# Performance work log

Measured on AMD Instinct MI355X. Metric: run time of the kernel, lower is better.

Reference implementation:

```python
import math
import jax, jax.numpy as jnp
import numpy as np

B, N, D, H = 4, 2048, 512, 8
HD = D // H


def setup_inputs() -> dict:
    key = jax.random.key(0)
    ks = jax.random.split(key, 7)
    w_scale = 1.0 / math.sqrt(D)  # keep logits in a sane range (like default init)
    return {
        "q": jax.random.normal(ks[0], (B, N, D), dtype=jnp.float32),
        "mask": jax.random.randint(ks[1], (B, N), 0, 2) == 1,  # True = masked key
        "attn_bias": jax.random.normal(ks[2], (B, N, N), dtype=jnp.float32),
        "Wq": jax.random.normal(ks[3], (D, D), dtype=jnp.float32) * w_scale,
        "Wk": jax.random.normal(ks[4], (D, D), dtype=jnp.float32) * w_scale,
        "Wv": jax.random.normal(ks[5], (D, D), dtype=jnp.float32) * w_scale,
        "Wo": jax.random.normal(ks[6], (D, D), dtype=jnp.float32) * w_scale,
    }


def _heads(v):
    # [B, N, D] -> [H, B, N, HD]  (mirrors reshape + movedim(-2, 0))
    b, n, d = v.shape
    return v.reshape(b, n, H, HD).transpose(2, 0, 1, 3)


def reference(q, mask, attn_bias, Wq, Wk, Wv, Wo):
    # Linear projections (torch Linear: x @ W.T)
    qh = _heads(q @ Wq.T)
    kh = _heads(q @ Wk.T)   # self-attention: h defaults to q
    vh = _heads(q @ Wv.T)
    # scores: [H, B, Nq, Nk]
    scores = jnp.einsum("hbqd,hbkd->hbqk", qh, kh) / math.sqrt(HD)
    scores = scores + attn_bias[None]                     # broadcast over heads
    scores = jnp.where(mask[None, :, None, :], -jnp.inf, scores)
    attn = jax.nn.softmax(scores, axis=-1)
    out = jnp.einsum("hbqk,hbkd->hbqd", attn, vh)         # [H, B, Nq, HD]
    out = out.transpose(1, 2, 0, 3).reshape(q.shape[0], q.shape[1], D)
    return out @ Wo.T
```

## Files before the change

kernel.cpp:

```cpp
#include <hip/hip_runtime.h>
#include <stdint.h>


typedef __attribute__((ext_vector_type(8))) short short8;
typedef __attribute__((ext_vector_type(4))) short short4v;
typedef __attribute__((ext_vector_type(4))) float f32x4;

#define DEV static __device__ __forceinline__

constexpr int Bc = 4, Nc = 2048, Dc = 512, Hc = 8, HDc = 64;
constexpr int Mc = Bc * Nc;
constexpr int QKVNc = 3 * Dc;
constexpr float L2E = 1.44269504f;

DEV short bf16cast(float f) {
  return (short)__builtin_bit_cast(unsigned short, (__bf16)f);
}
DEV unsigned cvt_pk_bf16(float a, float b) {
  unsigned short lb = __builtin_bit_cast(unsigned short, (__bf16)a);
  unsigned short hb = __builtin_bit_cast(unsigned short, (__bf16)b);
  return (unsigned)lb | ((unsigned)hb << 16);
}
DEV unsigned pack_shorts(short a, short b) {
  return (unsigned)(unsigned short)a | ((unsigned)(unsigned short)b << 16);
}
DEV short8 cvt8(float4 a, float4 b) {
  union { short8 s; uint4 u; } r;
  r.u.x = cvt_pk_bf16(a.x, a.y); r.u.y = cvt_pk_bf16(a.z, a.w);
  r.u.z = cvt_pk_bf16(b.x, b.y); r.u.w = cvt_pk_bf16(b.z, b.w);
  return r.s;
}
DEV float fast_exp2(float x) {
#if __has_builtin(__builtin_amdgcn_exp2f)
  return __builtin_amdgcn_exp2f(x);
#else
  return exp2f(x);
#endif
}
DEV void permswap32(unsigned& a, unsigned& b) {
  asm volatile("v_permlane32_swap_b32 %0, %1" : "+v"(a), "+v"(b));
}

__global__ void cvtw_kernel(const float* __restrict__ Wq, const float* __restrict__ Wk,
                            const float* __restrict__ Wv, const float* __restrict__ Wo,
                            short* __restrict__ Wqkv, short* __restrict__ Wob) {
  int which = blockIdx.x >> 8;
  int j = (blockIdx.x & 255) * 256 + threadIdx.x;
  const float* src = which == 0 ? Wq : which == 1 ? Wk : which == 2 ? Wv : Wo;
  short* dst = (which == 3) ? Wob : Wqkv + which * (Dc * Dc);
  float4 v = ((const float4*)src)[j];
  short4v o = { bf16cast(v.x), bf16cast(v.y), bf16cast(v.z), bf16cast(v.w) };
  ((short4v*)dst)[j] = o;
}

__global__ void maskprep_kernel(const void* __restrict__ mask, float* __restrict__ mf) {
  __shared__ int flag;
  if (threadIdx.x == 0) flag = 0;
  __syncthreads();
  const uchar4* m4 = (const uchar4*)mask;
  int acc = 0;
  for (int i = threadIdx.x; i < 2048; i += 1024) {
    uchar4 v = m4[i];
    acc |= (int)v.y | (int)v.z | (int)v.w;
  }
  if (acc) atomicOr(&flag, 1);
  __syncthreads();
  int isbyte = flag;
  for (int i = threadIdx.x; i < Bc * Nc; i += 1024) {
    int v = isbyte ? (int)((const unsigned char*)mask)[i] : ((const int*)mask)[i];
    mf[i] = v ? -1e30f : 0.0f;
  }
}

template<bool A_F32, bool OUT_F32>
__global__ __launch_bounds__(256, 2) void gemm_bt(const void* __restrict__ Av,
                                                  const short* __restrict__ Bm,
                                                  void* __restrict__ Cv,
                                                  int M, int N, int K,
                                                  int qcols, float cscale) {
  __shared__ __align__(16) short At[128 * 72];
  __shared__ __align__(16) short Bt[128 * 72];
  const int tid = threadIdx.x, lane = tid & 63, wv = tid >> 6;
  const int quad = lane >> 4, l16 = lane & 15;
  const int mbase = blockIdx.y * 128, nbase = blockIdx.x * 128;
  const int wr = (wv >> 1) * 64, wc = (wv & 1) * 64;
  const float scale = (nbase < qcols) ? cscale : 1.0f;
  f32x4 acc[4][4] = {};
  float4 apf[4][2]; short8 aph[4], bpre[4];
#pragma unroll
  for (int i = 0; i < 4; i++) {
    int flat = i * 256 + tid, row = flat >> 3, ch8 = (flat & 7) * 8;
    if (A_F32) {
      const float* Af = (const float*)Av;
      apf[i][0] = *(const float4*)&Af[(size_t)(mbase + row) * K + ch8];
      apf[i][1] = *(const float4*)&Af[(size_t)(mbase + row) * K + ch8 + 4];
    } else {
      aph[i] = *(const short8*)&((const short*)Av)[(size_t)(mbase + row) * K + ch8];
    }
    bpre[i] = *(const short8*)&Bm[(size_t)(nbase + row) * K + ch8];
  }
  for (int k0 = 0; k0 < K; k0 += 64) {
    __syncthreads();
#pragma unroll
    for (int i = 0; i < 4; i++) {
      int flat = i * 256 + tid, row = flat >> 3, ch8 = (flat & 7) * 8;
      *(short8*)&At[row * 72 + ch8] = A_F32 ? cvt8(apf[i][0], apf[i][1]) : aph[i];
      *(short8*)&Bt[row * 72 + ch8] = bpre[i];
    }
    if (k0 + 64 < K) {
#pragma unroll
      for (int i = 0; i < 4; i++) {
        int flat = i * 256 + tid, row = flat >> 3, ch8 = (flat & 7) * 8;
        if (A_F32) {
          const float* Af = (const float*)Av;
          apf[i][0] = *(const float4*)&Af[(size_t)(mbase + row) * K + k0 + 64 + ch8];
          apf[i][1] = *(const float4*)&Af[(size_t)(mbase + row) * K + k0 + 64 + ch8 + 4];
        } else {
          aph[i] = *(const short8*)&((const short*)Av)[(size_t)(mbase + row) * K + k0 + 64 + ch8];
        }
        bpre[i] = *(const short8*)&Bm[(size_t)(nbase + row) * K + k0 + 64 + ch8];
      }
    }
    __syncthreads();
#pragma unroll
    for (int s = 0; s < 2; s++) {
      short8 af[4], bf[4];
#pragma unroll
      for (int t = 0; t < 4; t++) {
        af[t] = *(short8*)&At[(wr + t * 16 + l16) * 72 + quad * 8 + s * 32];
        bf[t] = *(short8*)&Bt[(wc + t * 16 + l16) * 72 + quad * 8 + s * 32];
      }
#pragma unroll
      for (int mt = 0; mt < 4; mt++)
#pragma unroll
        for (int nt = 0; nt < 4; nt++)
          acc[mt][nt] = __builtin_amdgcn_mfma_f32_16x16x32_bf16(af[mt], bf[nt], acc[mt][nt], 0, 0, 0);
    }
  }
#pragma unroll
  for (int mt = 0; mt < 4; mt++)
#pragma unroll
    for (int nt = 0; nt < 4; nt++)
#pragma unroll
      for (int r = 0; r < 4; r++) {
        int row = mbase + wr + mt * 16 + quad * 4 + r;
        int col = nbase + wc + nt * 16 + l16;
        float v = acc[mt][nt][r] * scale;
        if (OUT_F32) ((float*)Cv)[(size_t)row * N + col] = v;
        else         ((short*)Cv)[(size_t)row * N + col] = bf16cast(v);
      }
}

__global__ __launch_bounds__(256, 2) void attn_kernel(const short* __restrict__ QKV,
                                                      const float* __restrict__ bias,
                                                      const float* __restrict__ maskf,
                                                      short* __restrict__ Aout) {
  __shared__ __align__(16) short Kt[2][64 * 64];
  __shared__ __align__(16) short Vt[2][64 * 64];
  __shared__ __align__(16) float mlds[Nc];
  const int tid = threadIdx.x, lane = tid & 63, wv = tid >> 6;
  const int quad = lane >> 4, l16 = lane & 15;
  const int qt = blockIdx.x & 15, h = (blockIdx.x >> 4) & 7, b = (int)(blockIdx.x >> 7);
  const int qrow0 = qt * 128;
  const int q0 = qrow0 + wv * 32 + l16;
  const float* biasq0 = bias + ((size_t)b * Nc + q0) * Nc;
  const float* biasq1 = biasq0 + (size_t)16 * Nc;

  ((float4*)mlds)[tid]       = ((const float4*)(maskf + b * Nc))[tid];
  ((float4*)mlds)[tid + 256] = ((const float4*)(maskf + b * Nc))[tid + 256];

  short8 qf[2][2];
  {
    const short* qp0 = QKV + (size_t)(b * Nc + q0) * QKVNc + h * HDc + quad * 8;
    qf[0][0] = *(const short8*)qp0;
    qf[0][1] = *(const short8*)(qp0 + 32);
    const short* qp1 = qp0 + (size_t)16 * QKVNc;
    qf[1][0] = *(const short8*)qp1;
    qf[1][1] = *(const short8*)(qp1 + 32);
  }

  const int krow = tid >> 2, kch0 = (tid & 3) * 2;
  const int kw0 = krow * 64 + ((kch0 ^ (krow & 7)) << 3);
  const int kw1 = krow * 64 + (((kch0 + 1) ^ (krow & 7)) << 3);
  const int vp = tid & 31, vq = tid >> 5;
  const int vperm = (vp & 25) | ((vp & 4) >> 1) | ((vp & 2) << 1);
  const int vwbase = (((vperm >> 2)) << 3) + 2 * (vperm & 3);
  const short* Kbase = QKV + Dc + h * HDc;
  const short* Vbase = QKV + 2 * Dc + h * HDc;

  short8 kpre0, kpre1, v0pre, v1pre;
  {
    const short* kp = &Kbase[(size_t)(b * Nc + krow) * QKVNc + kch0 * 8];
    kpre0 = *(const short8*)kp;
    kpre1 = *(const short8*)(kp + 8);
    v0pre = *(const short8*)&Vbase[(size_t)(b * Nc + 2 * vp) * QKVNc + vq * 8];
    v1pre = *(const short8*)&Vbase[(size_t)(b * Nc + 2 * vp + 1) * QKVNc + vq * 8];
  }

  const short ONEB = (short)0x3F80;
  const short8 ones = { ONEB, ONEB, ONEB, ONEB, ONEB, ONEB, ONEB, ONEB };

  f32x4 oacc[2][4] = {};
  f32x4 sumacc[2] = {};

  for (int kt = 0; kt < 32; kt++) {
    const int cur = kt & 1;
    const int kb = kt * 64;
    const int kbn = ((kt + 1) & 31) * 64;

    *(short8*)&Kt[cur][kw0] = kpre0;
    *(short8*)&Kt[cur][kw1] = kpre1;
#pragma unroll
    for (int j = 0; j < 8; j++) {
      int hd = vq * 8 + j;
      *(unsigned*)&Vt[cur][hd * 64 + (vwbase ^ ((hd & 7) << 3))] =
          pack_shorts(v0pre[j], v1pre[j]);
    }
    __syncthreads();

    {
      const short* kp = &Kbase[(size_t)(b * Nc + kbn + krow) * QKVNc + kch0 * 8];
      kpre0 = *(const short8*)kp;
      kpre1 = *(const short8*)(kp + 8);
      v0pre = *(const short8*)&Vbase[(size_t)(b * Nc + kbn + 2 * vp) * QKVNc + vq * 8];
      v1pre = *(const short8*)&Vbase[(size_t)(b * Nc + kbn + 2 * vp + 1) * QKVNc + vq * 8];
    }
    float4 bb[2][4];
#pragma unroll
    for (int t = 0; t < 4; t++) {
      bb[0][t] = *(const float4*)&biasq0[kb + t * 16 + quad * 4];
      bb[1][t] = *(const float4*)&biasq1[kb + t * 16 + quad * 4];
    }

    f32x4 sacc[2][4];
#pragma unroll
    for (int t = 0; t < 4; t++) {
      float4 mv = *(const float4*)&mlds[kb + t * 16 + quad * 4];
      sacc[0][t][0] = mv.x; sacc[0][t][1] = mv.y; sacc[0][t][2] = mv.z; sacc[0][t][3] = mv.w;
      sacc[1][t] = sacc[0][t];
    }

#pragma unroll
    for (int s = 0; s < 2; s++)
#pragma unroll
      for (int t = 0; t < 4; t++) {
        short8 kf = *(short8*)&Kt[cur][(t * 16 + l16) * 64 + (((quad + 4 * s) ^ (l16 & 7)) << 3)];
        sacc[0][t] = __builtin_amdgcn_mfma_f32_16x16x32_bf16(kf, qf[0][s], sacc[0][t], 0, 0, 0);
        sacc[1][t] = __builtin_amdgcn_mfma_f32_16x16x32_bf16(kf, qf[1][s], sacc[1][t], 0, 0, 0);
      }

    short8 pf[2][2];
#pragma unroll
    for (int n = 0; n < 2; n++) {
      unsigned pw[4][2];
#pragma unroll
      for (int t = 0; t < 4; t++) {
        float p0 = fast_exp2(__builtin_fmaf(bb[n][t].x, L2E, sacc[n][t][0]));
        float p1 = fast_exp2(__builtin_fmaf(bb[n][t].y, L2E, sacc[n][t][1]));
        float p2 = fast_exp2(__builtin_fmaf(bb[n][t].z, L2E, sacc[n][t][2]));
        float p3 = fast_exp2(__builtin_fmaf(bb[n][t].w, L2E, sacc[n][t][3]));
        pw[t][0] = cvt_pk_bf16(p0, p1);
        pw[t][1] = cvt_pk_bf16(p2, p3);
      }
      permswap32(pw[0][0], pw[1][0]); permswap32(pw[0][1], pw[1][1]);
      permswap32(pw[2][0], pw[3][0]); permswap32(pw[2][1], pw[3][1]);
      union { unsigned u[4]; short8 s; }
          a0{{pw[0][0], pw[0][1], pw[1][0], pw[1][1]}},
          a1{{pw[2][0], pw[2][1], pw[3][0], pw[3][1]}};
      pf[n][0] = a0.s; pf[n][1] = a1.s;
    }

#pragma unroll
    for (int s = 0; s < 2; s++) {
      sumacc[0] = __builtin_amdgcn_mfma_f32_16x16x32_bf16(pf[0][s], ones, sumacc[0], 0, 0, 0);
      sumacc[1] = __builtin_amdgcn_mfma_f32_16x16x32_bf16(pf[1][s], ones, sumacc[1], 0, 0, 0);
#pragma unroll
      for (int t = 0; t < 4; t++) {
        short8 vf = *(short8*)&Vt[cur][(t * 16 + l16) * 64 + (((quad + 4 * s) ^ (l16 & 7)) << 3)];
        oacc[0][t] = __builtin_amdgcn_mfma_f32_16x16x32_bf16(pf[0][s], vf, oacc[0][t], 0, 0, 0);
        oacc[1][t] = __builtin_amdgcn_mfma_f32_16x16x32_bf16(pf[1][s], vf, oacc[1][t], 0, 0, 0);
      }
    }
  }

#pragma unroll
  for (int m = 0; m < 2; m++)
#pragma unroll
    for (int r = 0; r < 4; r++) {
      float inv = 1.0f / sumacc[m][r];
      int row = b * Nc + qrow0 + wv * 32 + m * 16 + quad * 4 + r;
#pragma unroll
      for (int t = 0; t < 4; t++)
        Aout[(size_t)row * Dc + h * HDc + t * 16 + l16] = bf16cast(oacc[m][t][r] * inv);
    }
}

extern "C" void kernel_launch(void* const* d_in, const int* in_sizes, int n_in,
                              void* d_out, int out_size, void* d_ws, size_t ws_size,
                              hipStream_t stream) {
  const float* q    = (const float*)d_in[0];
  const void*  mask = d_in[1];
  const float* bias = (const float*)d_in[2];
  const float* Wq   = (const float*)d_in[3];
  const float* Wk   = (const float*)d_in[4];
  const float* Wv   = (const float*)d_in[5];
  const float* Wo   = (const float*)d_in[6];
  float* out = (float*)d_out;

  char* ws = (char*)d_ws;
  short* Wqkv = (short*)ws;  ws += (size_t)QKVNc * Dc * 2;
  short* Wob  = (short*)ws;  ws += (size_t)Dc * Dc * 2;
  float* mf   = (float*)ws;  ws += (size_t)Bc * Nc * 4;
  short* QKV  = (short*)ws;  ws += (size_t)Mc * QKVNc * 2;
  short* aout = (short*)ws;  ws += (size_t)Mc * Dc * 2;

  cvtw_kernel<<<dim3(1024), dim3(256), 0, stream>>>(Wq, Wk, Wv, Wo, Wqkv, Wob);
  maskprep_kernel<<<dim3(1), dim3(1024), 0, stream>>>(mask, mf);

  gemm_bt<true, false><<<dim3(QKVNc / 128, Mc / 128), dim3(256), 0, stream>>>(
      (const void*)q, Wqkv, (void*)QKV, Mc, QKVNc, Dc, Dc, 0.125f * L2E);
  attn_kernel<<<dim3(Bc * Hc * 16), dim3(256), 0, stream>>>(QKV, bias, mf, aout);
  gemm_bt<false, true><<<dim3(Dc / 128, Mc / 128), dim3(256), 0, stream>>>(
      (const void*)aout, Wob, (void*)out, Mc, Dc, Dc, 0, 1.0f);
}
```

Measured before the change: 273.0 us.

## Use direct global-to-LDS loads with XOR swizzle in GEMMs and prep-convert q

The GEMM now stages A and B tiles with global_load_lds directly into an XOR-swizzled, unpadded LDS layout, in place of register prefetch followed by LDS stores. To allow this, q is converted to bf16 in a merged prep kernel that also absorbs the mask preparation, removing one launch. The output projection uses a 128x64 tile with more waves per SIMD to raise occupancy and block count. In exchange, the register-level double buffering is gone, so each k-step now waits on its loads with no overlap, and converting q costs an extra pass through memory.

```diff
diff --git a/kernel.cpp b/kernel.cpp
--- a/kernel.cpp
+++ b/kernel.cpp
@@ -23,12 +23,6 @@
 }
 DEV unsigned pack_shorts(short a, short b) {
   return (unsigned)(unsigned short)a | ((unsigned)(unsigned short)b << 16);
-}
-DEV short8 cvt8(float4 a, float4 b) {
-  union { short8 s; uint4 u; } r;
-  r.u.x = cvt_pk_bf16(a.x, a.y); r.u.y = cvt_pk_bf16(a.z, a.w);
-  r.u.z = cvt_pk_bf16(b.x, b.y); r.u.w = cvt_pk_bf16(b.z, b.w);
-  return r.s;
 }
 DEV float fast_exp2(float x) {
 #if __has_builtin(__builtin_amdgcn_exp2f)
@@ -40,107 +34,112 @@
 DEV void permswap32(unsigned& a, unsigned& b) {
   asm volatile("v_permlane32_swap_b32 %0, %1" : "+v"(a), "+v"(b));
 }
+DEV void gl_lds16(const short* g, short* l) {
+  __builtin_amdgcn_global_load_lds(
+      (const __attribute__((address_space(1))) void*)g,
+      (__attribute__((address_space(3))) void*)l, 16, 0, 0);
+}
 
 __global__ void cvtw_kernel(const float* __restrict__ Wq, const float* __restrict__ Wk,
                             const float* __restrict__ Wv, const float* __restrict__ Wo,
-                            short* __restrict__ Wqkv, short* __restrict__ Wob) {
-  int which = blockIdx.x >> 8;
-  int j = (blockIdx.x & 255) * 256 + threadIdx.x;
-  const float* src = which == 0 ? Wq : which == 1 ? Wk : which == 2 ? Wv : Wo;
-  short* dst = (which == 3) ? Wob : Wqkv + which * (Dc * Dc);
+                            const float* __restrict__ q,
+                            short* __restrict__ Wqkv, short* __restrict__ Wob,
+                            short* __restrict__ qb,
+                            const void* __restrict__ mask, float* __restrict__ mf) {
+  int bid = blockIdx.x;
+  if (bid >= 5120) {
+    __shared__ int flag;
+    if (threadIdx.x == 0) flag = 0;
+    __syncthreads();
+    const uchar4* m4 = (const uchar4*)mask;
+    int acc = 0;
+    for (int i = threadIdx.x; i < 2048; i += 256) {
+      uchar4 v = m4[i];
+      acc |= (int)v.y | (int)v.z | (int)v.w;
+    }
+    if (acc) atomicOr(&flag, 1);
+    __syncthreads();
+    int isbyte = flag;
+    for (int i = threadIdx.x; i < Bc * Nc; i += 256) {
+      int v = isbyte ? (int)((const unsigned char*)mask)[i] : ((const int*)mask)[i];
+      mf[i] = v ? -1e30f : 0.0f;
+    }
+    return;
+  }
+  const float* src; short* dst; int j;
+  if (bid < 1024) {
+    int which = bid >> 8;
+    j = (bid & 255) * 256 + threadIdx.x;
+    src = which == 0 ? Wq : which == 1 ? Wk : which == 2 ? Wv : Wo;
+    dst = (which == 3) ? Wob : Wqkv + which * (Dc * Dc);
+  } else {
+    j = (bid - 1024) * 256 + threadIdx.x;
+    src = q; dst = qb;
+  }
   float4 v = ((const float4*)src)[j];
   short4v o = { bf16cast(v.x), bf16cast(v.y), bf16cast(v.z), bf16cast(v.w) };
   ((short4v*)dst)[j] = o;
 }
 
-__global__ void maskprep_kernel(const void* __restrict__ mask, float* __restrict__ mf) {
-  __shared__ int flag;
-  if (threadIdx.x == 0) flag = 0;
-  __syncthreads();
-  const uchar4* m4 = (const uchar4*)mask;
-  int acc = 0;
-  for (int i = threadIdx.x; i < 2048; i += 1024) {
-    uchar4 v = m4[i];
-    acc |= (int)v.y | (int)v.z | (int)v.w;
-  }
-  if (acc) atomicOr(&flag, 1);
-  __syncthreads();
-  int isbyte = flag;
-  for (int i = threadIdx.x; i < Bc * Nc; i += 1024) {
-    int v = isbyte ? (int)((const unsigned char*)mask)[i] : ((const int*)mask)[i];
-    mf[i] = v ? -1e30f : 0.0f;
-  }
-}
-
-template<bool A_F32, bool OUT_F32>
-__global__ __launch_bounds__(256, 2) void gemm_bt(const void* __restrict__ Av,
-                                                  const short* __restrict__ Bm,
-                                                  void* __restrict__ Cv,
-                                                  int M, int N, int K,
-                                                  int qcols, float cscale) {
-  __shared__ __align__(16) short At[128 * 72];
-  __shared__ __align__(16) short Bt[128 * 72];
+template<int BN, bool OUT_F32, int MINW>
+__global__ __launch_bounds__(256, MINW) void gemm_bt(const short* __restrict__ A,
+                                                     const short* __restrict__ Bm,
+                                                     void* __restrict__ Cv,
+                                                     int M, int N, int K,
+                                                     int qcols, float cscale) {
+  constexpr int MT = (BN == 128) ? 4 : 2;
+  constexpr int NT = 4;
+  __shared__ __align__(16) short At[128 * 64];
+  __shared__ __align__(16) short Bt[BN * 64];
   const int tid = threadIdx.x, lane = tid & 63, wv = tid >> 6;
   const int quad = lane >> 4, l16 = lane & 15;
-  const int mbase = blockIdx.y * 128, nbase = blockIdx.x * 128;
-  const int wr = (wv >> 1) * 64, wc = (wv & 1) * 64;
+  const int mbase = blockIdx.y * 128, nbase = blockIdx.x * BN;
+  const int wr = (BN == 128) ? (wv >> 1) * 64 : wv * 32;
+  const int wc = (BN == 128) ? (wv & 1) * 64 : 0;
   const float scale = (nbase < qcols) ? cscale : 1.0f;
-  f32x4 acc[4][4] = {};
-  float4 apf[4][2]; short8 aph[4], bpre[4];
-#pragma unroll
-  for (int i = 0; i < 4; i++) {
-    int flat = i * 256 + tid, row = flat >> 3, ch8 = (flat & 7) * 8;
-    if (A_F32) {
-      const float* Af = (const float*)Av;
-      apf[i][0] = *(const float4*)&Af[(size_t)(mbase + row) * K + ch8];
-      apf[i][1] = *(const float4*)&Af[(size_t)(mbase + row) * K + ch8 + 4];
-    } else {
-      aph[i] = *(const short8*)&((const short*)Av)[(size_t)(mbase + row) * K + ch8];
-    }
-    bpre[i] = *(const short8*)&Bm[(size_t)(nbase + row) * K + ch8];
-  }
+  f32x4 acc[MT][NT] = {};
+
   for (int k0 = 0; k0 < K; k0 += 64) {
-    __syncthreads();
 #pragma unroll
     for (int i = 0; i < 4; i++) {
-      int flat = i * 256 + tid, row = flat >> 3, ch8 = (flat & 7) * 8;
-      *(short8*)&At[row * 72 + ch8] = A_F32 ? cvt8(apf[i][0], apf[i][1]) : aph[i];
-      *(short8*)&Bt[row * 72 + ch8] = bpre[i];
-    }
-    if (k0 + 64 < K) {
-#pragma unroll
-      for (int i = 0; i < 4; i++) {
-        int flat = i * 256 + tid, row = flat >> 3, ch8 = (flat & 7) * 8;
-        if (A_F32) {
-          const float* Af = (const float*)Av;
-          apf[i][0] = *(const float4*)&Af[(size_t)(mbase + row) * K + k0 + 64 + ch8];
-          apf[i][1] = *(const float4*)&Af[(size_t)(mbase + row) * K + k0 + 64 + ch8 + 4];
-        } else {
-          aph[i] = *(const short8*)&((const short*)Av)[(size_t)(mbase + row) * K + k0 + 64 + ch8];
-        }
-        bpre[i] = *(const short8*)&Bm[(size_t)(nbase + row) * K + k0 + 64 + ch8];
-      }
+      int ibase = (wv * 4 + i) * 64;
+      int row = (ibase + lane) >> 3, c = lane & 7;
+      gl_lds16(&A[(size_t)(mbase + row) * K + k0 + ((c ^ (row & 7)) << 3)],
+               &At[ibase << 3]);
+    }
+#pragma unroll
+    for (int i = 0; i < BN / 32; i++) {
+      int ibase = (wv * (BN / 32) + i) * 64;
+      int row = (ibase + lane) >> 3, c = lane & 7;
+      gl_lds16(&Bm[(size_t)(nbase + row) * K + k0 + ((c ^ (row & 7)) << 3)],
+               &Bt[ibase << 3]);
     }
     __syncthreads();
 #pragma unroll
     for (int s = 0; s < 2; s++) {
-      short8 af[4], bf[4];
-#pragma unroll
-      for (int t = 0; t < 4; t++) {
-        af[t] = *(short8*)&At[(wr + t * 16 + l16) * 72 + quad * 8 + s * 32];
-        bf[t] = *(short8*)&Bt[(wc + t * 16 + l16) * 72 + quad * 8 + s * 32];
-      }
-#pragma unroll
-      for (int mt = 0; mt < 4; mt++)
-#pragma unroll
-        for (int nt = 0; nt < 4; nt++)
+      short8 af[MT], bf[NT];
+#pragma unroll
+      for (int t = 0; t < MT; t++) {
+        int r = wr + t * 16 + l16;
+        af[t] = *(short8*)&At[r * 64 + (((quad + 4 * s) ^ (r & 7)) << 3)];
+      }
+#pragma unroll
+      for (int t = 0; t < NT; t++) {
+        int r = wc + t * 16 + l16;
+        bf[t] = *(short8*)&Bt[r * 64 + (((quad + 4 * s) ^ (r & 7)) << 3)];
+      }
+#pragma unroll
+      for (int mt = 0; mt < MT; mt++)
+#pragma unroll
+        for (int nt = 0; nt < NT; nt++)
           acc[mt][nt] = __builtin_amdgcn_mfma_f32_16x16x32_bf16(af[mt], bf[nt], acc[mt][nt], 0, 0, 0);
     }
-  }
-#pragma unroll
-  for (int mt = 0; mt < 4; mt++)
-#pragma unroll
-    for (int nt = 0; nt < 4; nt++)
+    __syncthreads();
+  }
+#pragma unroll
+  for (int mt = 0; mt < MT; mt++)
+#pragma unroll
+    for (int nt = 0; nt < NT; nt++)
 #pragma unroll
       for (int r = 0; r < 4; r++) {
         int row = mbase + wr + mt * 16 + quad * 4 + r;
@@ -313,13 +312,13 @@
   float* mf   = (float*)ws;  ws += (size_t)Bc * Nc * 4;
   short* QKV  = (short*)ws;  ws += (size_t)Mc * QKVNc * 2;
   short* aout = (short*)ws;  ws += (size_t)Mc * Dc * 2;
-
-  cvtw_kernel<<<dim3(1024), dim3(256), 0, stream>>>(Wq, Wk, Wv, Wo, Wqkv, Wob);
-  maskprep_kernel<<<dim3(1), dim3(1024), 0, stream>>>(mask, mf);
-
-  gemm_bt<true, false><<<dim3(QKVNc / 128, Mc / 128), dim3(256), 0, stream>>>(
-      (const void*)q, Wqkv, (void*)QKV, Mc, QKVNc, Dc, Dc, 0.125f * L2E);
+  short* qb   = (short*)ws;  ws += (size_t)Mc * Dc * 2;
+
+  cvtw_kernel<<<dim3(5121), dim3(256), 0, stream>>>(Wq, Wk, Wv, Wo, q, Wqkv, Wob, qb, mask, mf);
+
+  gemm_bt<128, false, 3><<<dim3(QKVNc / 128, Mc / 128), dim3(256), 0, stream>>>(
+      qb, Wqkv, (void*)QKV, Mc, QKVNc, Dc, Dc, 0.125f * L2E);
   attn_kernel<<<dim3(Bc * Hc * 16), dim3(256), 0, stream>>>(QKV, bias, mf, aout);
-  gemm_bt<false, true><<<dim3(Dc / 128, Mc / 128), dim3(256), 0, stream>>>(
-      (const void*)aout, Wob, (void*)out, Mc, Dc, Dc, 0, 1.0f);
-}
+  gemm_bt<64, true, 4><<<dim3(Dc / 64, Mc / 128), dim3(256), 0, stream>>>(
+      aout, Wob, (void*)out, Mc, Dc, Dc, 0, 1.0f);
+}
```

After: 269.5 us. No clear change (-1.3%).
